# Performance work log

Hardware: AMD Instinct MI355X
Metric: run time of the kernel (lower is better)

## Reference

```python
import jax, jax.numpy as jnp
import numpy as np

N, NS, C, S = 262144, 8, 32, 8  # points, nsample, out_channels, share_channels
EPS = 1e-5

def _bn(x, g, b, axes):
    m = jnp.mean(x, axis=axes, keepdims=True)
    v = jnp.mean((x - m) ** 2, axis=axes, keepdims=True)
    return g * (x - m) * jax.lax.rsqrt(v + EPS) + b

def setup_inputs() -> dict:
    key = jax.random.key(0)
    ks = jax.random.split(key, 16)
    lin = lambda k, i, o: (jax.random.normal(k, (o, i), jnp.float32) / np.sqrt(i)).astype(jnp.float32)
    return {
        'p': jax.random.normal(ks[0], (N, 3), jnp.float32) * 10.0,
        'x': jax.random.normal(ks[1], (N, C), jnp.float32),
        'idx': jax.random.randint(ks[2], (N, NS), 0, N, jnp.int32),
        'Wq': lin(ks[3], C, C), 'bq': jnp.zeros((C,), jnp.float32),
        'Wk': lin(ks[4], C, C), 'bk': jnp.zeros((C,), jnp.float32),
        'Wv': lin(ks[5], C, C), 'bv': jnp.zeros((C,), jnp.float32),
        'Wp1': lin(ks[6], 3, 3), 'bp1': jnp.zeros((3,), jnp.float32),
        'gp': jnp.ones((3,), jnp.float32), 'bp': jnp.zeros((3,), jnp.float32),
        'Wp2': lin(ks[7], 3, C), 'bp2': jnp.zeros((C,), jnp.float32),
        'gw1': jnp.ones((C,), jnp.float32), 'bw1': jnp.zeros((C,), jnp.float32),
        'Ww1': lin(ks[8], C, C // S), 'bww1': jnp.zeros((C // S,), jnp.float32),
        'gw2': jnp.ones((C // S,), jnp.float32), 'bw2': jnp.zeros((C // S,), jnp.float32),
        'Ww2': lin(ks[9], C // S, C // S), 'bww2': jnp.zeros((C // S,), jnp.float32),
    }

def reference(p, x, idx, Wq, bq, Wk, bk, Wv, bv, Wp1, bp1, gp, bp, Wp2, bp2,
              gw1, bw1, Ww1, bww1, gw2, bw2, Ww2, bww2):
    n = x.shape[0]
    q = x @ Wq.T + bq                      # (n, C)
    k = x @ Wk.T + bk
    v = x @ Wv.T + bv
    # queryandgroup: gather neighbors, relative xyz (use_xyz=True for key path)
    p_r = p[idx] - p[:, None, :]           # (n, ns, 3)
    kg = k[idx]                            # (n, ns, C)
    vg = v[idx]                            # (n, ns, C)
    # linear_p: Linear(3,3) -> BN(3) (over n, ns) -> ReLU -> Linear(3, C)
    p_r = p_r @ Wp1.T + bp1
    p_r = jax.nn.relu(_bn(p_r, gp, bp, (0, 1)))
    p_r = p_r @ Wp2.T + bp2                # (n, ns, C)
    # out_channels // mid_channels == 1, so the .view(...).sum(2) is identity
    w = kg - q[:, None, :] + p_r           # (n, ns, C)
    # linear_w: BN(C) -> ReLU -> Linear(C, C//S) -> BN(C//S) -> ReLU -> Linear
    w = jax.nn.relu(_bn(w, gw1, bw1, (0, 1)))
    w = w @ Ww1.T + bww1                   # (n, ns, C//S)
    w = jax.nn.relu(_bn(w, gw2, bw2, (0, 1)))
    w = w @ Ww2.T + bww2
    w = jax.nn.softmax(w, axis=1)          # softmax over nsample
    # grouped weighted sum: (n, ns, S, C//S) * (n, ns, 1, C//S)
    out = ((vg + p_r).reshape(n, NS, S, C // S) * w[:, :, None, :]).sum(1)
    return out.reshape(n, C)
```

## Files before the change

kernel.cpp:

```cpp
#include <hip/hip_runtime.h>
#include <hip/hip_bf16.h>

#define NPTS   262144
#define NSAMP  8
#define NPAIR  (NPTS * NSAMP)
#define EPSV   1e-5f
#define INVCNT (1.0f / (float)NPAIR)
#define GSTAT  1024

typedef __hip_bfloat16 bf16;

template <typename T> __device__ __forceinline__ float cvt(T v);
template <> __device__ __forceinline__ float cvt<float>(float v) { return v; }
template <> __device__ __forceinline__ float cvt<bf16>(bf16 v) { return __bfloat162float(v); }

template <typename T> __device__ __forceinline__ T f2t(float v);
template <> __device__ __forceinline__ float f2t<float>(float v) { return v; }
template <> __device__ __forceinline__ bf16  f2t<bf16>(float v)  { return __float2bfloat16(v); }

__global__ void k_detect(const unsigned int* __restrict__ xw, int* __restrict__ flag)
{
    if (threadIdx.x == 0 && blockIdx.x == 0) {
        int cnt = 0;
        for (int i = 0; i < 256; ++i) {
            const unsigned int w = xw[i];
            const unsigned int e = (w >> 7) & 0xFF;
            if (e >= 110 && e <= 132) ++cnt;
        }
        flag[0] = (cnt >= 128) ? 0 : 1;
    }
}

template <typename T>
__global__ __launch_bounds__(256) void k_qkv(
    const T* __restrict__ x,
    const T* __restrict__ Wq, const T* __restrict__ bq,
    const T* __restrict__ Wk, const T* __restrict__ bk,
    const T* __restrict__ Wv, const T* __restrict__ bv,
    float* __restrict__ q, float* __restrict__ k, float* __restrict__ v,
    const int* __restrict__ flag, const int want)
{
    if (flag[0] != want) return;
    __shared__ float Wt[3][32][32];
    __shared__ float xs[8][32];
    const int t = threadIdx.x;
    for (int e = t; e < 1024; e += 256) {
        const int c = e >> 5, j = e & 31;
        Wt[0][j][c] = cvt<T>(Wq[e]);
        Wt[1][j][c] = cvt<T>(Wk[e]);
        Wt[2][j][c] = cvt<T>(Wv[e]);
    }
    __syncthreads();
    const int c = t & 31, pi = t >> 5;
    const float bqv = cvt<T>(bq[c]), bkv = cvt<T>(bk[c]), bvv = cvt<T>(bv[c]);
    const int base0 = blockIdx.x * 256;
    for (int it = 0; it < 32; ++it) {
        const int base = base0 + it * 8;
        __syncthreads();
        xs[t >> 5][t & 31] = cvt<T>(x[base * 32 + t]);
        __syncthreads();
        float aq = bqv, ak = bkv, av = bvv;
#pragma unroll
        for (int j = 0; j < 32; ++j) {
            const float xv = xs[pi][j];
            aq += Wt[0][j][c] * xv;
            ak += Wt[1][j][c] * xv;
            av += Wt[2][j][c] * xv;
        }
        const int o = (base + pi) * 32 + c;
        q[o] = aq; k[o] = ak; v[o] = av;
    }
}

template <typename T>
__global__ __launch_bounds__(256) void k_pr1(
    const T* __restrict__ p, const int* __restrict__ idx,
    const T* __restrict__ Wp1, const T* __restrict__ bp1,
    float* __restrict__ pr1, float* __restrict__ P1,
    const int* __restrict__ flag, const int want)
{
    if (flag[0] != want) return;
    float W[3][3], B[3];
#pragma unroll
    for (int a = 0; a < 3; ++a) {
        B[a] = cvt<T>(bp1[a]);
#pragma unroll
        for (int d = 0; d < 3; ++d) W[a][d] = cvt<T>(Wp1[a * 3 + d]);
    }
    const int t = threadIdx.x;
    const int base = blockIdx.x * 2048;
    float s[3] = {0.f, 0.f, 0.f}, ss[3] = {0.f, 0.f, 0.f};
    for (int it = 0; it < 2048; it += 256) {
        const int pid = base + it + t;
        const int i = pid >> 3;
        const int nj = idx[pid];
        const float d0 = cvt<T>(p[nj * 3 + 0]) - cvt<T>(p[i * 3 + 0]);
        const float d1 = cvt<T>(p[nj * 3 + 1]) - cvt<T>(p[i * 3 + 1]);
        const float d2 = cvt<T>(p[nj * 3 + 2]) - cvt<T>(p[i * 3 + 2]);
#pragma unroll
        for (int a = 0; a < 3; ++a) {
            const float r = W[a][0] * d0 + W[a][1] * d1 + W[a][2] * d2 + B[a];
            pr1[pid * 3 + a] = r;
            s[a] += r; ss[a] += r * r;
        }
    }
#pragma unroll
    for (int o = 32; o > 0; o >>= 1) {
#pragma unroll
        for (int a = 0; a < 3; ++a) { s[a] += __shfl_down(s[a], o); ss[a] += __shfl_down(ss[a], o); }
    }
    __shared__ float red[4][16];
    const int wid = t >> 6, lane = t & 63;
    if (lane == 0) {
#pragma unroll
        for (int u = 0; u < 16; ++u) red[wid][u] = 0.f;
#pragma unroll
        for (int a = 0; a < 3; ++a) { red[wid][a] = s[a]; red[wid][8 + a] = ss[a]; }
    }
    __syncthreads();
    if (t < 16) P1[blockIdx.x * 16 + t] = red[0][t] + red[1][t] + red[2][t] + red[3][t];
}

template <typename T, int NC_, int NP_>
__global__ __launch_bounds__(1024) void k_fin(
    const float* __restrict__ P, const int nblocks,
    const T* __restrict__ g, const T* __restrict__ b,
    float* __restrict__ A, float* __restrict__ Cc,
    const int* __restrict__ flag, const int want)
{
    if (flag[0] != want) return;
    constexpr int COLS = 2 * NP_;
    constexpr int GRP  = 1024 / COLS;
    const int t = threadIdx.x;
    const int c = t % COLS;
    const int gi = t / COLS;
    float acc = 0.f;
    for (int r = gi; r < nblocks; r += GRP) acc += P[r * COLS + c];
    __shared__ float red[1024];
    red[t] = acc;
    __syncthreads();
#pragma unroll
    for (int s = GRP >> 1; s > 0; s >>= 1) {
        if (gi < s) red[t] += red[t + s * COLS];
        __syncthreads();
    }
    if (t < NC_) {
        const float m = red[t] * INVCNT;
        const float var = red[NP_ + t] * INVCNT - m * m;
        const float a = cvt<T>(g[t]) * rsqrtf(var + EPSV);
        A[t] = a;
        Cc[t] = cvt<T>(b[t]) - a * m;
    }
}

template <typename T>
__global__ __launch_bounds__(256) void k_bn2stat(
    const int* __restrict__ idx, const float* __restrict__ pr1,
    const float* __restrict__ q, const float* __restrict__ k,
    const T* __restrict__ Wp2, const T* __restrict__ bp2,
    const float* __restrict__ coef, float* __restrict__ P2,
    const int* __restrict__ flag, const int want)
{
    if (flag[0] != want) return;
    const int t = threadIdx.x;
    const int c = t & 31;
    const float a10 = coef[0], a11 = coef[1], a12 = coef[2];
    const float c10 = coef[8], c11 = coef[9], c12 = coef[10];
    const float w0 = cvt<T>(Wp2[c * 3 + 0]), w1 = cvt<T>(Wp2[c * 3 + 1]), w2 = cvt<T>(Wp2[c * 3 + 2]);
    const float bb = cvt<T>(bp2[c]);
    float s = 0.f, ss = 0.f;
    const int base = blockIdx.x * 2048;
    for (int it = 0; it < 2048; it += 8) {
        const int pid = base + it + (t >> 5);
        const int i = pid >> 3;
        const int nj = idx[pid];
        const float h0 = fmaxf(a10 * pr1[pid * 3 + 0] + c10, 0.f);
        const float h1 = fmaxf(a11 * pr1[pid * 3 + 1] + c11, 0.f);
        const float h2 = fmaxf(a12 * pr1[pid * 3 + 2] + c12, 0.f);
        const float pr2 = w0 * h0 + w1 * h1 + w2 * h2 + bb;
        const float wp = k[nj * 32 + c] - q[i * 32 + c] + pr2;
        s += wp; ss += wp * wp;
    }
    s += __shfl_down(s, 32); ss += __shfl_down(ss, 32);
    __shared__ float red[4][64];
    const int wid = t >> 6, lane = t & 63;
    if (lane < 32) { red[wid][lane] = s; red[wid][32 + lane] = ss; }
    __syncthreads();
    if (t < 64) P2[blockIdx.x * 64 + t] = red[0][t] + red[1][t] + red[2][t] + red[3][t];
}

template <typename T>
__global__ __launch_bounds__(256) void k_w1(
    const int* __restrict__ idx, const float* __restrict__ pr1,
    const float* __restrict__ q, const float* __restrict__ k,
    const T* __restrict__ Wp2, const T* __restrict__ bp2,
    const T* __restrict__ Ww1, const T* __restrict__ bww1,
    const float* __restrict__ coef, float* __restrict__ w1out, float* __restrict__ P3,
    const int* __restrict__ flag, const int want)
{
    if (flag[0] != want) return;
    __shared__ float sWp2[32][3], sbp2[32], sW1[4][32], sb1[4], sa2[32], sc2[32];
    const int t = threadIdx.x;
    if (t < 32) {
        sWp2[t][0] = cvt<T>(Wp2[t * 3 + 0]);
        sWp2[t][1] = cvt<T>(Wp2[t * 3 + 1]);
        sWp2[t][2] = cvt<T>(Wp2[t * 3 + 2]);
        sbp2[t] = cvt<T>(bp2[t]);
        sa2[t] = coef[16 + t];
        sc2[t] = coef[48 + t];
    }
    if (t < 4) sb1[t] = cvt<T>(bww1[t]);
    if (t < 128) sW1[t >> 5][t & 31] = cvt<T>(Ww1[t]);
    __syncthreads();
    const float a10 = coef[0], a11 = coef[1], a12 = coef[2];
    const float c10 = coef[8], c11 = coef[9], c12 = coef[10];
    float s[4] = {0.f, 0.f, 0.f, 0.f}, ss[4] = {0.f, 0.f, 0.f, 0.f};
    const int base = blockIdx.x * 2048;
    for (int it = 0; it < 2048; it += 256) {
        const int pid = base + it + t;
        const int i = pid >> 3;
        const int nj = idx[pid];
        const float h0 = fmaxf(a10 * pr1[pid * 3 + 0] + c10, 0.f);
        const float h1 = fmaxf(a11 * pr1[pid * 3 + 1] + c11, 0.f);
        const float h2 = fmaxf(a12 * pr1[pid * 3 + 2] + c12, 0.f);
        float acc[4] = {sb1[0], sb1[1], sb1[2], sb1[3]};
        const float* krow = k + nj * 32;
        const float* qrow = q + i * 32;
#pragma unroll
        for (int cc = 0; cc < 32; ++cc) {
            const float pr2 = sWp2[cc][0] * h0 + sWp2[cc][1] * h1 + sWp2[cc][2] * h2 + sbp2[cc];
            const float wp = krow[cc] - qrow[cc] + pr2;
            const float hh = fmaxf(sa2[cc] * wp + sc2[cc], 0.f);
            acc[0] += sW1[0][cc] * hh;
            acc[1] += sW1[1][cc] * hh;
            acc[2] += sW1[2][cc] * hh;
            acc[3] += sW1[3][cc] * hh;
        }
#pragma unroll
        for (int u = 0; u < 4; ++u) {
            w1out[pid * 4 + u] = acc[u];
            s[u] += acc[u]; ss[u] += acc[u] * acc[u];
        }
    }
#pragma unroll
    for (int o = 32; o > 0; o >>= 1) {
#pragma unroll
        for (int u = 0; u < 4; ++u) { s[u] += __shfl_down(s[u], o); ss[u] += __shfl_down(ss[u], o); }
    }
    __shared__ float red[4][8];
    const int wid = t >> 6, lane = t & 63;
    if (lane == 0) {
#pragma unroll
        for (int u = 0; u < 4; ++u) { red[wid][u] = s[u]; red[wid][4 + u] = ss[u]; }
    }
    __syncthreads();
    if (t < 8) P3[blockIdx.x * 8 + t] = red[0][t] + red[1][t] + red[2][t] + red[3][t];
}

template <typename T>
__global__ __launch_bounds__(256) void k_out(
    const int* __restrict__ idx, const float* __restrict__ pr1,
    const float* __restrict__ v, const float* __restrict__ w1in,
    const T* __restrict__ Wp2, const T* __restrict__ bp2,
    const T* __restrict__ Ww2, const T* __restrict__ bww2,
    const float* __restrict__ coef, T* __restrict__ out,
    const int* __restrict__ flag, const int want)
{
    if (flag[0] != want) return;
    const int t = threadIdx.x;
    const int c = t & 31, pi = t >> 5;
    const float a10 = coef[0], a11 = coef[1], a12 = coef[2];
    const float c10 = coef[8], c11 = coef[9], c12 = coef[10];
    const float wA = cvt<T>(Wp2[c * 3 + 0]), wB = cvt<T>(Wp2[c * 3 + 1]), wC = cvt<T>(Wp2[c * 3 + 2]);
    const float bb = cvt<T>(bp2[c]);
    const int tq = c & 3;
    float a3[4], c3[4], W2r[4];
#pragma unroll
    for (int u = 0; u < 4; ++u) {
        a3[u] = coef[80 + u]; c3[u] = coef[88 + u];
        W2r[u] = cvt<T>(Ww2[tq * 4 + u]);
    }
    const float b2r = cvt<T>(bww2[tq]);
    const int base0 = blockIdx.x * 256;
    for (int it = 0; it < 32; ++it) {
        const int i = base0 + it * 8 + pi;
        float lg[8];
#pragma unroll
        for (int j = 0; j < 8; ++j) {
            const float* wr = w1in + (i * 8 + j) * 4;
            float l = b2r;
#pragma unroll
            for (int u = 0; u < 4; ++u) l += W2r[u] * fmaxf(a3[u] * wr[u] + c3[u], 0.f);
            lg[j] = l;
        }
        float m = lg[0];
#pragma unroll
        for (int j = 1; j < 8; ++j) m = fmaxf(m, lg[j]);
        float sum = 0.f;
#pragma unroll
        for (int j = 0; j < 8; ++j) { lg[j] = __expf(lg[j] - m); sum += lg[j]; }
        const float inv = 1.f / sum;
        float acc = 0.f;
#pragma unroll
        for (int j = 0; j < 8; ++j) {
            const int pid = i * 8 + j;
            const int nj = idx[pid];
            const float h0 = fmaxf(a10 * pr1[pid * 3 + 0] + c10, 0.f);
            const float h1 = fmaxf(a11 * pr1[pid * 3 + 1] + c11, 0.f);
            const float h2 = fmaxf(a12 * pr1[pid * 3 + 2] + c12, 0.f);
            const float pr2 = wA * h0 + wB * h1 + wC * h2 + bb;
            acc += (v[nj * 32 + c] + pr2) * (lg[j] * inv);
        }
        out[i * 32 + c] = f2t<T>(acc);
    }
}

template <typename T>
static void launch_pipeline(void* const* d_in, void* d_out, float* ws,
                            int* flag, const int want, hipStream_t stream)
{
    const T*   p    = (const T*)d_in[0];
    const T*   x    = (const T*)d_in[1];
    const int* idx  = (const int*)d_in[2];
    const T*   Wq   = (const T*)d_in[3];
    const T*   bq   = (const T*)d_in[4];
    const T*   Wk   = (const T*)d_in[5];
    const T*   bk   = (const T*)d_in[6];
    const T*   Wv   = (const T*)d_in[7];
    const T*   bv   = (const T*)d_in[8];
    const T*   Wp1  = (const T*)d_in[9];
    const T*   bp1  = (const T*)d_in[10];
    const T*   gp   = (const T*)d_in[11];
    const T*   bp   = (const T*)d_in[12];
    const T*   Wp2  = (const T*)d_in[13];
    const T*   bp2  = (const T*)d_in[14];
    const T*   gw1  = (const T*)d_in[15];
    const T*   bw1  = (const T*)d_in[16];
    const T*   Ww1  = (const T*)d_in[17];
    const T*   bww1 = (const T*)d_in[18];
    const T*   gw2  = (const T*)d_in[19];
    const T*   bw2  = (const T*)d_in[20];
    const T*   Ww2  = (const T*)d_in[21];
    const T*   bww2 = (const T*)d_in[22];
    T* out = (T*)d_out;

    float* coef = ws + 16;
    float* P1   = ws + 128;
    float* P2   = P1 + GSTAT * 16;
    float* P3   = P2 + GSTAT * 64;
    float* q    = ws + 131072;
    float* k    = q  + (size_t)NPTS * 32;
    float* v    = k  + (size_t)NPTS * 32;
    float* pr1  = v  + (size_t)NPTS * 32;
    float* w1   = pr1 + (size_t)NPAIR * 3;

    k_qkv<T><<<1024, 256, 0, stream>>>(x, Wq, bq, Wk, bk, Wv, bv, q, k, v, flag, want);
    k_pr1<T><<<GSTAT, 256, 0, stream>>>(p, idx, Wp1, bp1, pr1, P1, flag, want);
    k_fin<T, 3, 8><<<1, 1024, 0, stream>>>(P1, GSTAT, gp, bp, coef + 0, coef + 8, flag, want);
    k_bn2stat<T><<<GSTAT, 256, 0, stream>>>(idx, pr1, q, k, Wp2, bp2, coef, P2, flag, want);
    k_fin<T, 32, 32><<<1, 1024, 0, stream>>>(P2, GSTAT, gw1, bw1, coef + 16, coef + 48, flag, want);
    k_w1<T><<<GSTAT, 256, 0, stream>>>(idx, pr1, q, k, Wp2, bp2, Ww1, bww1, coef, w1, P3, flag, want);
    k_fin<T, 4, 4><<<1, 1024, 0, stream>>>(P3, GSTAT, gw2, bw2, coef + 80, coef + 88, flag, want);
    k_out<T><<<1024, 256, 0, stream>>>(idx, pr1, v, w1, Wp2, bp2, Ww2, bww2, coef, out, flag, want);
}

extern "C" void kernel_launch(void* const* d_in, const int* in_sizes, int n_in,
                              void* d_out, int out_size, void* d_ws, size_t ws_size,
                              hipStream_t stream)
{
    float* ws = (float*)d_ws;
    int* flag = (int*)ws;

    k_detect<<<1, 64, 0, stream>>>((const unsigned int*)d_in[1], flag);
    launch_pipeline<bf16>(d_in, d_out, ws, flag, 0, stream);
    launch_pipeline<float>(d_in, d_out, ws, flag, 1, stream);
}
```

Baseline: 521.8 us.

## Double grid sizes, parallelize BN finalization per channel, atomically merge P2 partials

Every main pass now launches twice as many blocks, each doing half the work, to improve occupancy and load balance across CUs. The BN-finalize kernel now uses one 256-thread block per channel with wavefront shuffle reductions, replacing a single 1024-thread block with a shared-memory tree. The bn2stat partials are merged pairwise with atomicAdd into a buffer that k_qkv zeroes first, which keeps the row count the finalizer reads unchanged. In exchange, float accumulation order becomes nondeterministic and there are more per-block setup and reduction overheads.

New measurement: 488.5 us. -6.4%, faster.

```diff
diff --git a/kernel.cpp b/kernel.cpp
--- a/kernel.cpp
+++ b/kernel.cpp
@@ -6,7 +6,8 @@
 #define NPAIR  (NPTS * NSAMP)
 #define EPSV   1e-5f
 #define INVCNT (1.0f / (float)NPAIR)
-#define GSTAT  1024
+#define GSTAT  2048
+#define P2ROWS 1024
 
 typedef __hip_bfloat16 bf16;
 
@@ -38,12 +39,14 @@
     const T* __restrict__ Wk, const T* __restrict__ bk,
     const T* __restrict__ Wv, const T* __restrict__ bv,
     float* __restrict__ q, float* __restrict__ k, float* __restrict__ v,
+    float* __restrict__ P2z,
     const int* __restrict__ flag, const int want)
 {
     if (flag[0] != want) return;
     __shared__ float Wt[3][32][32];
     __shared__ float xs[8][32];
     const int t = threadIdx.x;
+    if (t < 32) P2z[blockIdx.x * 32 + t] = 0.f;
     for (int e = t; e < 1024; e += 256) {
         const int c = e >> 5, j = e & 31;
         Wt[0][j][c] = cvt<T>(Wq[e]);
@@ -53,8 +56,8 @@
     __syncthreads();
     const int c = t & 31, pi = t >> 5;
     const float bqv = cvt<T>(bq[c]), bkv = cvt<T>(bk[c]), bvv = cvt<T>(bv[c]);
-    const int base0 = blockIdx.x * 256;
-    for (int it = 0; it < 32; ++it) {
+    const int base0 = blockIdx.x * 128;
+    for (int it = 0; it < 16; ++it) {
         const int base = base0 + it * 8;
         __syncthreads();
         xs[t >> 5][t & 31] = cvt<T>(x[base * 32 + t]);
@@ -88,9 +91,9 @@
         for (int d = 0; d < 3; ++d) W[a][d] = cvt<T>(Wp1[a * 3 + d]);
     }
     const int t = threadIdx.x;
-    const int base = blockIdx.x * 2048;
+    const int base = blockIdx.x * 1024;
     float s[3] = {0.f, 0.f, 0.f}, ss[3] = {0.f, 0.f, 0.f};
-    for (int it = 0; it < 2048; it += 256) {
+    for (int it = 0; it < 1024; it += 256) {
         const int pid = base + it + t;
         const int i = pid >> 3;
         const int nj = idx[pid];
@@ -122,34 +125,34 @@
 }
 
 template <typename T, int NC_, int NP_>
-__global__ __launch_bounds__(1024) void k_fin(
-    const float* __restrict__ P, const int nblocks,
+__global__ __launch_bounds__(256) void k_fin(
+    const float* __restrict__ P, const int nrows,
     const T* __restrict__ g, const T* __restrict__ b,
     float* __restrict__ A, float* __restrict__ Cc,
     const int* __restrict__ flag, const int want)
 {
     if (flag[0] != want) return;
     constexpr int COLS = 2 * NP_;
-    constexpr int GRP  = 1024 / COLS;
-    const int t = threadIdx.x;
-    const int c = t % COLS;
-    const int gi = t / COLS;
-    float acc = 0.f;
-    for (int r = gi; r < nblocks; r += GRP) acc += P[r * COLS + c];
-    __shared__ float red[1024];
-    red[t] = acc;
-    __syncthreads();
-#pragma unroll
-    for (int s = GRP >> 1; s > 0; s >>= 1) {
-        if (gi < s) red[t] += red[t + s * COLS];
-        __syncthreads();
-    }
-    if (t < NC_) {
-        const float m = red[t] * INVCNT;
-        const float var = red[NP_ + t] * INVCNT - m * m;
-        const float a = cvt<T>(g[t]) * rsqrtf(var + EPSV);
-        A[t] = a;
-        Cc[t] = cvt<T>(b[t]) - a * m;
+    const int c = blockIdx.x;
+    const int t = threadIdx.x;
+    float s = 0.f, ss = 0.f;
+    for (int r = t; r < nrows; r += 256) {
+        s  += P[r * COLS + c];
+        ss += P[r * COLS + NP_ + c];
+    }
+#pragma unroll
+    for (int o = 32; o > 0; o >>= 1) { s += __shfl_down(s, o); ss += __shfl_down(ss, o); }
+    __shared__ float rs[4], rss[4];
+    if ((t & 63) == 0) { rs[t >> 6] = s; rss[t >> 6] = ss; }
+    __syncthreads();
+    if (t == 0) {
+        s  = rs[0] + rs[1] + rs[2] + rs[3];
+        ss = rss[0] + rss[1] + rss[2] + rss[3];
+        const float m = s * INVCNT;
+        const float var = ss * INVCNT - m * m;
+        const float a = cvt<T>(g[c]) * rsqrtf(var + EPSV);
+        A[c]  = a;
+        Cc[c] = cvt<T>(b[c]) - a * m;
     }
 }
 
@@ -169,8 +172,8 @@
     const float w0 = cvt<T>(Wp2[c * 3 + 0]), w1 = cvt<T>(Wp2[c * 3 + 1]), w2 = cvt<T>(Wp2[c * 3 + 2]);
     const float bb = cvt<T>(bp2[c]);
     float s = 0.f, ss = 0.f;
-    const int base = blockIdx.x * 2048;
-    for (int it = 0; it < 2048; it += 8) {
+    const int base = blockIdx.x * 1024;
+    for (int it = 0; it < 1024; it += 8) {
         const int pid = base + it + (t >> 5);
         const int i = pid >> 3;
         const int nj = idx[pid];
@@ -186,7 +189,8 @@
     const int wid = t >> 6, lane = t & 63;
     if (lane < 32) { red[wid][lane] = s; red[wid][32 + lane] = ss; }
     __syncthreads();
-    if (t < 64) P2[blockIdx.x * 64 + t] = red[0][t] + red[1][t] + red[2][t] + red[3][t];
+    if (t < 64) atomicAdd(&P2[(blockIdx.x >> 1) * 64 + t],
+                          red[0][t] + red[1][t] + red[2][t] + red[3][t]);
 }
 
 template <typename T>
@@ -215,8 +219,8 @@
     const float a10 = coef[0], a11 = coef[1], a12 = coef[2];
     const float c10 = coef[8], c11 = coef[9], c12 = coef[10];
     float s[4] = {0.f, 0.f, 0.f, 0.f}, ss[4] = {0.f, 0.f, 0.f, 0.f};
-    const int base = blockIdx.x * 2048;
-    for (int it = 0; it < 2048; it += 256) {
+    const int base = blockIdx.x * 1024;
+    for (int it = 0; it < 1024; it += 256) {
         const int pid = base + it + t;
         const int i = pid >> 3;
         const int nj = idx[pid];
@@ -281,8 +285,8 @@
         W2r[u] = cvt<T>(Ww2[tq * 4 + u]);
     }
     const float b2r = cvt<T>(bww2[tq]);
-    const int base0 = blockIdx.x * 256;
-    for (int it = 0; it < 32; ++it) {
+    const int base0 = blockIdx.x * 128;
+    for (int it = 0; it < 16; ++it) {
         const int i = base0 + it * 8 + pi;
         float lg[8];
 #pragma unroll
@@ -347,21 +351,21 @@
     float* coef = ws + 16;
     float* P1   = ws + 128;
     float* P2   = P1 + GSTAT * 16;
-    float* P3   = P2 + GSTAT * 64;
+    float* P3   = P2 + P2ROWS * 64;
     float* q    = ws + 131072;
     float* k    = q  + (size_t)NPTS * 32;
     float* v    = k  + (size_t)NPTS * 32;
     float* pr1  = v  + (size_t)NPTS * 32;
     float* w1   = pr1 + (size_t)NPAIR * 3;
 
-    k_qkv<T><<<1024, 256, 0, stream>>>(x, Wq, bq, Wk, bk, Wv, bv, q, k, v, flag, want);
+    k_qkv<T><<<2048, 256, 0, stream>>>(x, Wq, bq, Wk, bk, Wv, bv, q, k, v, P2, flag, want);
     k_pr1<T><<<GSTAT, 256, 0, stream>>>(p, idx, Wp1, bp1, pr1, P1, flag, want);
-    k_fin<T, 3, 8><<<1, 1024, 0, stream>>>(P1, GSTAT, gp, bp, coef + 0, coef + 8, flag, want);
+    k_fin<T, 3, 8><<<3, 256, 0, stream>>>(P1, GSTAT, gp, bp, coef + 0, coef + 8, flag, want);
     k_bn2stat<T><<<GSTAT, 256, 0, stream>>>(idx, pr1, q, k, Wp2, bp2, coef, P2, flag, want);
-    k_fin<T, 32, 32><<<1, 1024, 0, stream>>>(P2, GSTAT, gw1, bw1, coef + 16, coef + 48, flag, want);
+    k_fin<T, 32, 32><<<32, 256, 0, stream>>>(P2, P2ROWS, gw1, bw1, coef + 16, coef + 48, flag, want);
     k_w1<T><<<GSTAT, 256, 0, stream>>>(idx, pr1, q, k, Wp2, bp2, Ww1, bww1, coef, w1, P3, flag, want);
-    k_fin<T, 4, 4><<<1, 1024, 0, stream>>>(P3, GSTAT, gw2, bw2, coef + 80, coef + 88, flag, want);
-    k_out<T><<<1024, 256, 0, stream>>>(idx, pr1, v, w1, Wp2, bp2, Ww2, bww2, coef, out, flag, want);
+    k_fin<T, 4, 4><<<4, 256, 0, stream>>>(P3, GSTAT, gw2, bw2, coef + 80, coef + 88, flag, want);
+    k_out<T><<<2048, 256, 0, stream>>>(idx, pr1, v, w1, Wp2, bp2, Ww2, bww2, coef, out, flag, want);
 }
 
 extern "C" void kernel_launch(void* const* d_in, const int* in_sizes, int n_in,
```
